# Performance work log

Measured on AMD Instinct MI355X. Metric: run time of the kernel, lower is better.

Reference implementation:

```python
import jax, jax.numpy as jnp
import numpy as np

K_BITS = 8
MOMENTUM = 0.125
EPS = 1e-05


def linear_quant(x, bits=K_BITS):
    """Dynamic-range fake quantization (LinearQuantFunction with dynamic=True).

    max_ = max(|x.max()|, |x.min()|), min_ = -max_, so zero_point = quant_max/2
    exactly, and nudged_zero_point = round(quant_max/2) (banker's rounding, as
    in Python's round()).
    """
    qmax = (1 << bits) - 1
    mx = jnp.maximum(jnp.abs(jnp.max(x)), jnp.abs(jnp.min(x)))
    scale = (2.0 * mx) / qmax  # range / quant_max
    nzp = float(round(qmax / 2))  # nudged zero point (constant under dynamic symmetric range)
    nmin = -nzp * scale
    nmax = (qmax - nzp) * scale
    safe = jnp.where(scale == 0, 1.0, scale)  # range==0 -> passthrough
    cs = jnp.clip(x, nmin, nmax) - nmin
    q = jnp.floor(cs / safe + 0.5) * safe + nmin
    return jnp.where(scale == 0, x, q)


def setup_inputs() -> dict:
    key = jax.random.key(0)
    k1, k2 = jax.random.split(key)
    N, C, H, W = 64, 256, 56, 56
    x = jax.random.normal(k1, (N, C, H, W), dtype=jnp.float32)
    weight = jax.random.uniform(k2, (C,), dtype=jnp.float32) - 0.5  # reset_parameters: U[0,1)-0.5
    bias = jnp.zeros((C,), dtype=jnp.float32)
    run_mean = jnp.zeros((C,), dtype=jnp.float32)
    run_var = jnp.ones((C,), dtype=jnp.float32)
    return {"x": x, "weight": weight, "bias": bias, "run_mean": run_mean, "run_var": run_var}


def reference(x, weight, bias, run_mean, run_var):
    # Training-mode forward of QuantizedBatchNorm (k=8 -> linear_quant path).
    q = linear_quant
    m = MOMENTUM
    bc = lambda v: v[None, :, None, None]  # per-channel broadcast over [N,C,H,W]

    # batch mean over all axes except channel (== _reorg(input).mean(1))
    new_mean = jnp.mean(x, axis=(0, 2, 3))
    mean = q((1.0 - m) * run_mean + m * new_mean)  # quantized updated running mean
    ctr = q(x - bc(mean))

    new_var = jnp.mean(ctr * ctr, axis=(0, 2, 3))
    var = q((1.0 - m) * run_var + m * new_var)  # quantized updated running var

    # quantizing the broadcast tensor == quantizing the per-channel vector,
    # since the quant scale depends only on the global max magnitude
    inv_den = q(jnp.sqrt(var + EPS))
    xn = q(ctr / bc(inv_den))

    qw = q(weight)
    qb = q(bias)  # bias==0 -> range 0 -> passthrough
    y = q(bc(qw) * xn + bc(qb))
    return y
```

## Files before the change

kernel.cpp:

```cpp
#include <hip/hip_runtime.h>
#include <stdint.h>


#define C_CH 256
#define P4 784
#define PLANE_STRIDE 200704
#define NHW_F 200704.0f
#define NHW_D 200704.0
#define TOLB 1e-3f

typedef float natf4 __attribute__((ext_vector_type(4)));

__device__ __forceinline__ float fq(float x, float sc, float qn, float qx) {
  if (sc == 0.0f) return x;
  float cs = __fsub_rn(fminf(fmaxf(x, qn), qx), qn);
  float f  = floorf(__fadd_rn(__fdiv_rn(cs, sc), 0.5f));
  return __fadd_rn(__fmul_rn(f, sc), qn);
}

__device__ __forceinline__ void qparams(float amax, float& sc, float& qn, float& qx) {
  sc = __fdiv_rn(__fmul_rn(2.0f, amax), 255.0f);
  qn = __fmul_rn(-128.0f, sc);
  qx = __fmul_rn(127.0f, sc);
}

__device__ __forceinline__ float block_max(float v, float* buf4) {
  #pragma unroll
  for (int m = 1; m <= 32; m <<= 1) v = fmaxf(v, __shfl_xor(v, m, 64));
  if ((threadIdx.x & 63) == 0) buf4[threadIdx.x >> 6] = v;
  __syncthreads();
  float r = fmaxf(fmaxf(buf4[0], buf4[1]), fmaxf(buf4[2], buf4[3]));
  __syncthreads();
  return r;
}

__device__ __forceinline__ uint32_t qlevel(float xv, float r2, float c2,
    float m, float s1, float n1, float x1) {
  float q = fmaf(xv, r2, c2);
  q = fminf(fmaxf(q, 0.0f), 255.0f);
  const float qh = __fadd_rn(q, 0.5f);
  float fl = floorf(qh);
  const float d = __fsub_rn(qh, fl);
  if (__builtin_expect(fminf(d, __fsub_rn(1.0f, d)) < TOLB, 0)) {
    const float tt = __fsub_rn(xv, m);
    const float cs = __fsub_rn(fminf(fmaxf(tt, n1), x1), n1);
    fl = floorf(__fadd_rn(__fdiv_rn(cs, s1), 0.5f));
  }
  return (uint32_t)fl;
}

struct S1Out { float meanc, tmax, tmin, s1, n1, x1; };

__device__ __forceinline__ void s1_compute(const float* __restrict__ psum,
    const float* __restrict__ pmin, const float* __restrict__ pmax,
    const float* __restrict__ run_mean, float* buf4, S1Out& o) {
  const int t = threadIdx.x;
  float sum = __fadd_rn(__fadd_rn(__fadd_rn(psum[4*t], psum[4*t+1]), psum[4*t+2]), psum[4*t+3]);
  float mn = fminf(fminf(pmin[4*t], pmin[4*t+1]), fminf(pmin[4*t+2], pmin[4*t+3]));
  float mx = fmaxf(fmaxf(pmax[4*t], pmax[4*t+1]), fmaxf(pmax[4*t+2], pmax[4*t+3]));
  const float new_mean = __fdiv_rn(sum, NHW_F);
  const float mp = __fadd_rn(__fmul_rn(0.875f, run_mean[t]), __fmul_rn(0.125f, new_mean));
  const float am = block_max(fabsf(mp), buf4);
  float scm, qnm, qxm; qparams(am, scm, qnm, qxm);
  o.meanc = fq(mp, scm, qnm, qxm);
  o.tmax = __fsub_rn(mx, o.meanc);
  o.tmin = __fsub_rn(mn, o.meanc);
  const float a1 = block_max(fmaxf(fabsf(o.tmax), fabsf(o.tmin)), buf4);
  qparams(a1, o.s1, o.n1, o.x1);
}

__global__ __launch_bounds__(256) void k_p1(const float4* __restrict__ x4,
    float* __restrict__ psum, float* __restrict__ pmin, float* __restrict__ pmax) {
  const int c = blockIdx.x, s = blockIdx.y, t = threadIdx.x;
  const int B0 = (s * 16 * C_CH + c) * P4;
  float sum = 0.0f, mn = INFINITY, mx = -INFINITY;
  #pragma unroll 1
  for (int g = 0; g < 7; ++g) {
    float4 v[7];
    #pragma unroll
    for (int j = 0; j < 7; ++j) {
      const int u = t + 256 * (7 * g + j);
      v[j] = x4[B0 + (u / P4) * PLANE_STRIDE + (u % P4)];
    }
    #pragma unroll
    for (int j = 0; j < 7; ++j) {
      const float4 w = v[j];
      sum = __fadd_rn(sum, __fadd_rn(__fadd_rn(w.x, w.y), __fadd_rn(w.z, w.w)));
      mn = fminf(mn, fminf(fminf(w.x, w.y), fminf(w.z, w.w)));
      mx = fmaxf(mx, fmaxf(fmaxf(w.x, w.y), fmaxf(w.z, w.w)));
    }
  }
  #pragma unroll
  for (int m = 1; m <= 32; m <<= 1) {
    sum = __fadd_rn(sum, __shfl_xor(sum, m, 64));
    mn = fminf(mn, __shfl_xor(mn, m, 64));
    mx = fmaxf(mx, __shfl_xor(mx, m, 64));
  }
  __shared__ float red[12];
  const int w_ = t >> 6;
  if ((t & 63) == 0) { red[w_] = sum; red[4 + w_] = mn; red[8 + w_] = mx; }
  __syncthreads();
  if (t == 0) {
    const int idx = c * 4 + s;
    psum[idx] = __fadd_rn(__fadd_rn(__fadd_rn(red[0], red[1]), red[2]), red[3]);
    pmin[idx] = fminf(fminf(red[4], red[5]), fminf(red[6], red[7]));
    pmax[idx] = fmaxf(fmaxf(red[8], red[9]), fmaxf(red[10], red[11]));
  }
}

__global__ __launch_bounds__(256) void k_p2(const float4* __restrict__ x4,
    const float* __restrict__ psum, const float* __restrict__ pmin,
    const float* __restrict__ pmax, const float* __restrict__ run_mean,
    uint32_t* __restrict__ pk, uint32_t* __restrict__ pk2) {
  __shared__ float buf4[4];
  __shared__ float bc[1];
  const int c = blockIdx.x, s = blockIdx.y, t = threadIdx.x;
  S1Out o; s1_compute(psum, pmin, pmax, run_mean, buf4, o);
  if (t == c) bc[0] = o.meanc;
  __syncthreads();
  const float m_c = bc[0];
  const double rd = 1.0 / (double)o.s1;
  const float r2 = (float)rd;
  const float c2 = (float)((-(double)m_c - (double)o.n1) * rd);
  const int B0 = (s * 16 * C_CH + c) * P4;
  int sk = 0, sk2 = 0;
  #pragma unroll 1
  for (int g = 0; g < 7; ++g) {
    float4 v[7];
    #pragma unroll
    for (int j = 0; j < 7; ++j) {
      const int u = t + 256 * (7 * g + j);
      v[j] = x4[B0 + (u / P4) * PLANE_STRIDE + (u % P4)];
    }
    #pragma unroll
    for (int j = 0; j < 7; ++j) {
      const float4 w = v[j];
      const float vv[4] = {w.x, w.y, w.z, w.w};
      #pragma unroll
      for (int e = 0; e < 4; ++e) {
        const uint32_t k = qlevel(vv[e], r2, c2, m_c, o.s1, o.n1, o.x1);
        sk += (int)k; sk2 += (int)(k * k);
      }
    }
  }
  #pragma unroll
  for (int m = 1; m <= 32; m <<= 1) {
    sk += __shfl_xor(sk, m, 64);
    sk2 += __shfl_xor(sk2, m, 64);
  }
  __shared__ uint32_t ired[8];
  const int w_ = t >> 6;
  if ((t & 63) == 0) { ired[w_] = (uint32_t)sk; ired[4 + w_] = (uint32_t)sk2; }
  __syncthreads();
  if (t == 0) {
    const int idx = c * 4 + s;
    pk[idx]  = ired[0] + ired[1] + ired[2] + ired[3];
    pk2[idx] = ired[4] + ired[5] + ired[6] + ired[7];
  }
}

__global__ __launch_bounds__(256) void k_p3(const float4* __restrict__ x4,
    const float* __restrict__ psum, const float* __restrict__ pmin,
    const float* __restrict__ pmax, const uint32_t* __restrict__ pk,
    const uint32_t* __restrict__ pk2,
    const float* __restrict__ run_mean, const float* __restrict__ run_var,
    const float* __restrict__ weight, const float* __restrict__ bias,
    natf4* __restrict__ y4) {
  __shared__ float buf4[4];
  __shared__ float bc[4];
  __shared__ float lut[256];
  const int c = blockIdx.x, s = blockIdx.y, t = threadIdx.x;
  S1Out o; s1_compute(psum, pmin, pmax, run_mean, buf4, o);
  const unsigned long long ssq = (unsigned long long)pk2[4*t] + pk2[4*t+1]
                               + pk2[4*t+2] + pk2[4*t+3];
  const unsigned int skc = pk[4*t] + pk[4*t+1] + pk[4*t+2] + pk[4*t+3];
  const double s1d = (double)o.s1;
  const double sum_ctr2 = s1d * s1d *
      ((double)ssq - 256.0 * (double)skc + 16384.0 * NHW_D);
  const float new_var = (float)(sum_ctr2 / NHW_D);
  const float vp = __fadd_rn(__fmul_rn(0.875f, run_var[t]), __fmul_rn(0.125f, new_var));
  const float av = block_max(fabsf(vp), buf4);
  float scv, qnv, qxv; qparams(av, scv, qnv, qxv);
  const float varc = fq(vp, scv, qnv, qxv);
  const float dp = __fsqrt_rn(__fadd_rn(varc, 1e-5f));
  const float ad = block_max(fabsf(dp), buf4);
  float scd, qnd, qxd; qparams(ad, scd, qnd, qxd);
  const float idc = fq(dp, scd, qnd, qxd);
  const float ctrmax = fq(o.tmax, o.s1, o.n1, o.x1);
  const float ctrmin = fq(o.tmin, o.s1, o.n1, o.x1);
  const float xpmax = __fdiv_rn(ctrmax, idc);
  const float xpmin = __fdiv_rn(ctrmin, idc);
  const float a3 = block_max(fmaxf(fabsf(xpmax), fabsf(xpmin)), buf4);
  float s3, n3, x3; qparams(a3, s3, n3, x3);
  const float xnmax = fq(xpmax, s3, n3, x3);
  const float xnmin = fq(xpmin, s3, n3, x3);
  const float wv = weight[t];
  const float aw = block_max(fabsf(wv), buf4);
  float scw, qnw, qxw; qparams(aw, scw, qnw, qxw);
  const float qw = fq(wv, scw, qnw, qxw);
  const float bv = bias[t];
  const float ab = block_max(fabsf(bv), buf4);
  float scb, qnb, qxb; qparams(ab, scb, qnb, qxb);
  const float qb = fq(bv, scb, qnb, qxb);
  const float e1 = __fadd_rn(__fmul_rn(qw, xnmax), qb);
  const float e2 = __fadd_rn(__fmul_rn(qw, xnmin), qb);
  const float a4 = block_max(fmaxf(fabsf(e1), fabsf(e2)), buf4);
  float s4, n4, x4q; qparams(a4, s4, n4, x4q);
  if (t == c) { bc[0] = idc; bc[1] = qw; bc[2] = qb; bc[3] = o.meanc; }
  __syncthreads();
  const float idc_c = bc[0], qw_c = bc[1], qb_c = bc[2], m_c = bc[3];
  {
    const float ctr_t = __fadd_rn(__fmul_rn((float)t, o.s1), o.n1);
    const float xn_t = fq(__fdiv_rn(ctr_t, idc_c), s3, n3, x3);
    lut[t] = fq(__fadd_rn(__fmul_rn(qw_c, xn_t), qb_c), s4, n4, x4q);
  }
  __syncthreads();

  const double rd = 1.0 / (double)o.s1;
  const float r2 = (float)rd;
  const float c2 = (float)((-(double)m_c - (double)o.n1) * rd);
  const int B0 = (s * 16 * C_CH + c) * P4;
  const float4* x4v = (const float4*)x4;
  #pragma unroll 1
  for (int g = 0; g < 7; ++g) {
    float4 v[7]; int idx[7];
    #pragma unroll
    for (int j = 0; j < 7; ++j) {
      const int u = t + 256 * (7 * g + j);
      idx[j] = B0 + (u / P4) * PLANE_STRIDE + (u % P4);
      v[j] = x4v[idx[j]];
    }
    #pragma unroll
    for (int j = 0; j < 7; ++j) {
      const float4 w = v[j];
      natf4 out;
      out.x = lut[qlevel(w.x, r2, c2, m_c, o.s1, o.n1, o.x1)];
      out.y = lut[qlevel(w.y, r2, c2, m_c, o.s1, o.n1, o.x1)];
      out.z = lut[qlevel(w.z, r2, c2, m_c, o.s1, o.n1, o.x1)];
      out.w = lut[qlevel(w.w, r2, c2, m_c, o.s1, o.n1, o.x1)];
      __builtin_nontemporal_store(out, &y4[idx[j]]);
    }
  }
}

extern "C" void kernel_launch(void* const* d_in, const int* in_sizes, int n_in,
                              void* d_out, int out_size, void* d_ws, size_t ws_size,
                              hipStream_t stream) {
  const float4* x4      = (const float4*)d_in[0];
  const float* weight   = (const float*)d_in[1];
  const float* bias     = (const float*)d_in[2];
  const float* run_mean = (const float*)d_in[3];
  const float* run_var  = (const float*)d_in[4];
  natf4* y4 = (natf4*)d_out;

  float* w = (float*)d_ws;
  float* psum = w;
  float* pmin = w + 1024;
  float* pmax = w + 2048;
  uint32_t* pk  = (uint32_t*)(w + 3072);
  uint32_t* pk2 = (uint32_t*)(w + 4096);

  dim3 grid(C_CH, 4), blk(256);
  k_p1<<<grid, blk, 0, stream>>>(x4, psum, pmin, pmax);
  k_p2<<<grid, blk, 0, stream>>>(x4, psum, pmin, pmax, run_mean, pk, pk2);
  k_p3<<<grid, blk, 0, stream>>>(x4, psum, pmin, pmax, pk, pk2,
                                 run_mean, run_var, weight, bias, y4);
}
```

Before: 134.6 us.

## Cache 8-bit quantization levels in workspace so the final pass skips re-reading x

The second pass now packs each element's 8-bit quantization level into a byte buffer in the workspace. The third pass reads these bytes and looks up the LUT instead of re-reading the fp32 input and recomputing qlevel. This replaces a 4-byte read per element in the last pass with a 1-byte write in pass 2 and a 1-byte read in pass 3, cutting total memory traffic. It needs about 51 MB of extra workspace and changes the loop mapping to 16 elements per thread slot.

```diff
diff --git a/kernel.cpp b/kernel.cpp
--- a/kernel.cpp
+++ b/kernel.cpp
@@ -4,7 +4,9 @@
 
 #define C_CH 256
 #define P4 784
+#define P16 196
 #define PLANE_STRIDE 200704
+#define KPLANE_STRIDE 50176
 #define NHW_F 200704.0f
 #define NHW_D 200704.0
 #define TOLB 1e-3f
@@ -69,108 +71,11 @@
   qparams(a1, o.s1, o.n1, o.x1);
 }
 
-__global__ __launch_bounds__(256) void k_p1(const float4* __restrict__ x4,
-    float* __restrict__ psum, float* __restrict__ pmin, float* __restrict__ pmax) {
-  const int c = blockIdx.x, s = blockIdx.y, t = threadIdx.x;
-  const int B0 = (s * 16 * C_CH + c) * P4;
-  float sum = 0.0f, mn = INFINITY, mx = -INFINITY;
-  #pragma unroll 1
-  for (int g = 0; g < 7; ++g) {
-    float4 v[7];
-    #pragma unroll
-    for (int j = 0; j < 7; ++j) {
-      const int u = t + 256 * (7 * g + j);
-      v[j] = x4[B0 + (u / P4) * PLANE_STRIDE + (u % P4)];
-    }
-    #pragma unroll
-    for (int j = 0; j < 7; ++j) {
-      const float4 w = v[j];
-      sum = __fadd_rn(sum, __fadd_rn(__fadd_rn(w.x, w.y), __fadd_rn(w.z, w.w)));
-      mn = fminf(mn, fminf(fminf(w.x, w.y), fminf(w.z, w.w)));
-      mx = fmaxf(mx, fmaxf(fmaxf(w.x, w.y), fmaxf(w.z, w.w)));
-    }
-  }
-  #pragma unroll
-  for (int m = 1; m <= 32; m <<= 1) {
-    sum = __fadd_rn(sum, __shfl_xor(sum, m, 64));
-    mn = fminf(mn, __shfl_xor(mn, m, 64));
-    mx = fmaxf(mx, __shfl_xor(mx, m, 64));
-  }
-  __shared__ float red[12];
-  const int w_ = t >> 6;
-  if ((t & 63) == 0) { red[w_] = sum; red[4 + w_] = mn; red[8 + w_] = mx; }
-  __syncthreads();
-  if (t == 0) {
-    const int idx = c * 4 + s;
-    psum[idx] = __fadd_rn(__fadd_rn(__fadd_rn(red[0], red[1]), red[2]), red[3]);
-    pmin[idx] = fminf(fminf(red[4], red[5]), fminf(red[6], red[7]));
-    pmax[idx] = fmaxf(fmaxf(red[8], red[9]), fmaxf(red[10], red[11]));
-  }
-}
-
-__global__ __launch_bounds__(256) void k_p2(const float4* __restrict__ x4,
-    const float* __restrict__ psum, const float* __restrict__ pmin,
-    const float* __restrict__ pmax, const float* __restrict__ run_mean,
-    uint32_t* __restrict__ pk, uint32_t* __restrict__ pk2) {
-  __shared__ float buf4[4];
-  __shared__ float bc[1];
-  const int c = blockIdx.x, s = blockIdx.y, t = threadIdx.x;
-  S1Out o; s1_compute(psum, pmin, pmax, run_mean, buf4, o);
-  if (t == c) bc[0] = o.meanc;
-  __syncthreads();
-  const float m_c = bc[0];
-  const double rd = 1.0 / (double)o.s1;
-  const float r2 = (float)rd;
-  const float c2 = (float)((-(double)m_c - (double)o.n1) * rd);
-  const int B0 = (s * 16 * C_CH + c) * P4;
-  int sk = 0, sk2 = 0;
-  #pragma unroll 1
-  for (int g = 0; g < 7; ++g) {
-    float4 v[7];
-    #pragma unroll
-    for (int j = 0; j < 7; ++j) {
-      const int u = t + 256 * (7 * g + j);
-      v[j] = x4[B0 + (u / P4) * PLANE_STRIDE + (u % P4)];
-    }
-    #pragma unroll
-    for (int j = 0; j < 7; ++j) {
-      const float4 w = v[j];
-      const float vv[4] = {w.x, w.y, w.z, w.w};
-      #pragma unroll
-      for (int e = 0; e < 4; ++e) {
-        const uint32_t k = qlevel(vv[e], r2, c2, m_c, o.s1, o.n1, o.x1);
-        sk += (int)k; sk2 += (int)(k * k);
-      }
-    }
-  }
-  #pragma unroll
-  for (int m = 1; m <= 32; m <<= 1) {
-    sk += __shfl_xor(sk, m, 64);
-    sk2 += __shfl_xor(sk2, m, 64);
-  }
-  __shared__ uint32_t ired[8];
-  const int w_ = t >> 6;
-  if ((t & 63) == 0) { ired[w_] = (uint32_t)sk; ired[4 + w_] = (uint32_t)sk2; }
-  __syncthreads();
-  if (t == 0) {
-    const int idx = c * 4 + s;
-    pk[idx]  = ired[0] + ired[1] + ired[2] + ired[3];
-    pk2[idx] = ired[4] + ired[5] + ired[6] + ired[7];
-  }
-}
-
-__global__ __launch_bounds__(256) void k_p3(const float4* __restrict__ x4,
-    const float* __restrict__ psum, const float* __restrict__ pmin,
-    const float* __restrict__ pmax, const uint32_t* __restrict__ pk,
-    const uint32_t* __restrict__ pk2,
-    const float* __restrict__ run_mean, const float* __restrict__ run_var,
-    const float* __restrict__ weight, const float* __restrict__ bias,
-    natf4* __restrict__ y4) {
-  __shared__ float buf4[4];
-  __shared__ float bc[4];
-  __shared__ float lut[256];
-  const int c = blockIdx.x, s = blockIdx.y, t = threadIdx.x;
-  S1Out o; s1_compute(psum, pmin, pmax, run_mean, buf4, o);
+__device__ __forceinline__ void s2_and_lut(const S1Out& o,
+    const uint32_t* __restrict__ pk, const uint32_t* __restrict__ pk2,
+    const float* __restrict__ run_var, const float* __restrict__ weight,
+    const float* __restrict__ bias, float* buf4, float* bc, float* lut, int c) {
+  const int t = threadIdx.x;
   const unsigned long long ssq = (unsigned long long)pk2[4*t] + pk2[4*t+1]
                                + pk2[4*t+2] + pk2[4*t+3];
   const unsigned int skc = pk[4*t] + pk[4*t+1] + pk[4*t+2] + pk[4*t+3];
@@ -206,39 +111,190 @@
   const float e2 = __fadd_rn(__fmul_rn(qw, xnmin), qb);
   const float a4 = block_max(fmaxf(fabsf(e1), fabsf(e2)), buf4);
   float s4, n4, x4q; qparams(a4, s4, n4, x4q);
-  if (t == c) { bc[0] = idc; bc[1] = qw; bc[2] = qb; bc[3] = o.meanc; }
-  __syncthreads();
-  const float idc_c = bc[0], qw_c = bc[1], qb_c = bc[2], m_c = bc[3];
-  {
-    const float ctr_t = __fadd_rn(__fmul_rn((float)t, o.s1), o.n1);
-    const float xn_t = fq(__fdiv_rn(ctr_t, idc_c), s3, n3, x3);
-    lut[t] = fq(__fadd_rn(__fmul_rn(qw_c, xn_t), qb_c), s4, n4, x4q);
-  }
-  __syncthreads();
-
+  if (t == c) { bc[0] = idc; bc[1] = qw; bc[2] = qb; }
+  __syncthreads();
+  const float idc_c = bc[0], qw_c = bc[1], qb_c = bc[2];
+  const float ctr_t = __fadd_rn(__fmul_rn((float)t, o.s1), o.n1);
+  const float xn_t = fq(__fdiv_rn(ctr_t, idc_c), s3, n3, x3);
+  lut[t] = fq(__fadd_rn(__fmul_rn(qw_c, xn_t), qb_c), s4, n4, x4q);
+  __syncthreads();
+}
+
+__global__ __launch_bounds__(256) void k_p1(const float4* __restrict__ x4,
+    float* __restrict__ psum, float* __restrict__ pmin, float* __restrict__ pmax) {
+  const int c = blockIdx.x, s = blockIdx.y, t = threadIdx.x;
+  const int B0 = (s * 16 * C_CH + c) * P4;
+  float sum = 0.0f, mn = INFINITY, mx = -INFINITY;
+  #pragma unroll 1
+  for (int g = 0; g < 7; ++g) {
+    float4 v[7];
+    #pragma unroll
+    for (int j = 0; j < 7; ++j) {
+      const int u = t + 256 * (7 * g + j);
+      v[j] = x4[B0 + (u / P4) * PLANE_STRIDE + (u % P4)];
+    }
+    #pragma unroll
+    for (int j = 0; j < 7; ++j) {
+      const float4 w = v[j];
+      sum = __fadd_rn(sum, __fadd_rn(__fadd_rn(w.x, w.y), __fadd_rn(w.z, w.w)));
+      mn = fminf(mn, fminf(fminf(w.x, w.y), fminf(w.z, w.w)));
+      mx = fmaxf(mx, fmaxf(fmaxf(w.x, w.y), fmaxf(w.z, w.w)));
+    }
+  }
+  #pragma unroll
+  for (int m = 1; m <= 32; m <<= 1) {
+    sum = __fadd_rn(sum, __shfl_xor(sum, m, 64));
+    mn = fminf(mn, __shfl_xor(mn, m, 64));
+    mx = fmaxf(mx, __shfl_xor(mx, m, 64));
+  }
+  __shared__ float red[12];
+  const int w_ = t >> 6;
+  if ((t & 63) == 0) { red[w_] = sum; red[4 + w_] = mn; red[8 + w_] = mx; }
+  __syncthreads();
+  if (t == 0) {
+    const int idx = c * 4 + s;
+    psum[idx] = __fadd_rn(__fadd_rn(__fadd_rn(red[0], red[1]), red[2]), red[3]);
+    pmin[idx] = fminf(fminf(red[4], red[5]), fminf(red[6], red[7]));
+    pmax[idx] = fmaxf(fmaxf(red[8], red[9]), fmaxf(red[10], red[11]));
+  }
+}
+
+__global__ __launch_bounds__(256) void k_p2(const float4* __restrict__ x4,
+    uint4* __restrict__ kq4,
+    const float* __restrict__ psum, const float* __restrict__ pmin,
+    const float* __restrict__ pmax, const float* __restrict__ run_mean,
+    uint32_t* __restrict__ pk, uint32_t* __restrict__ pk2) {
+  __shared__ float buf4[4];
+  __shared__ float bc[1];
+  const int c = blockIdx.x, s = blockIdx.y, t = threadIdx.x;
+  S1Out o; s1_compute(psum, pmin, pmax, run_mean, buf4, o);
+  if (t == c) bc[0] = o.meanc;
+  __syncthreads();
+  const float m_c = bc[0];
   const double rd = 1.0 / (double)o.s1;
   const float r2 = (float)rd;
   const float c2 = (float)((-(double)m_c - (double)o.n1) * rd);
   const int B0 = (s * 16 * C_CH + c) * P4;
-  const float4* x4v = (const float4*)x4;
+  const int KB0 = (s * 16 * C_CH + c) * P16;
+  int sk = 0, sk2 = 0;
   #pragma unroll 1
-  for (int g = 0; g < 7; ++g) {
-    float4 v[7]; int idx[7];
-    #pragma unroll
-    for (int j = 0; j < 7; ++j) {
-      const int u = t + 256 * (7 * g + j);
-      idx[j] = B0 + (u / P4) * PLANE_STRIDE + (u % P4);
-      v[j] = x4v[idx[j]];
-    }
-    #pragma unroll
-    for (int j = 0; j < 7; ++j) {
-      const float4 w = v[j];
+  for (int mm = 0; mm < 6; ++mm) {
+    float4 v[8]; int pl[2], sl[2];
+    #pragma unroll
+    for (int h = 0; h < 2; ++h) {
+      const int g = t + 256 * (2 * mm + h);
+      pl[h] = g / P16; sl[h] = g - pl[h] * P16;
+      const float4* p = x4 + B0 + pl[h] * PLANE_STRIDE + 4 * sl[h];
+      v[4*h+0] = p[0]; v[4*h+1] = p[1]; v[4*h+2] = p[2]; v[4*h+3] = p[3];
+    }
+    #pragma unroll
+    for (int h = 0; h < 2; ++h) {
+      uint32_t kw[4];
+      #pragma unroll
+      for (int q = 0; q < 4; ++q) {
+        const float4 w = v[4*h+q];
+        const float vv[4] = {w.x, w.y, w.z, w.w};
+        uint32_t acc = 0;
+        #pragma unroll
+        for (int e = 0; e < 4; ++e) {
+          const uint32_t k = qlevel(vv[e], r2, c2, m_c, o.s1, o.n1, o.x1);
+          sk += (int)k; sk2 += (int)(k * k);
+          acc |= k << (8 * e);
+        }
+        kw[q] = acc;
+      }
+      uint4 st; st.x = kw[0]; st.y = kw[1]; st.z = kw[2]; st.w = kw[3];
+      kq4[KB0 + pl[h] * KPLANE_STRIDE + sl[h]] = st;
+    }
+  }
+  if (t < 64) {
+    const int g = 3072 + t;
+    const int plane = g / P16, slot = g - plane * P16;
+    const float4* p = x4 + B0 + plane * PLANE_STRIDE + 4 * slot;
+    uint32_t kw[4];
+    #pragma unroll
+    for (int q = 0; q < 4; ++q) {
+      const float4 w = p[q];
+      const float vv[4] = {w.x, w.y, w.z, w.w};
+      uint32_t acc = 0;
+      #pragma unroll
+      for (int e = 0; e < 4; ++e) {
+        const uint32_t k = qlevel(vv[e], r2, c2, m_c, o.s1, o.n1, o.x1);
+        sk += (int)k; sk2 += (int)(k * k);
+        acc |= k << (8 * e);
+      }
+      kw[q] = acc;
+    }
+    uint4 st; st.x = kw[0]; st.y = kw[1]; st.z = kw[2]; st.w = kw[3];
+    kq4[KB0 + plane * KPLANE_STRIDE + slot] = st;
+  }
+  #pragma unroll
+  for (int m = 1; m <= 32; m <<= 1) {
+    sk += __shfl_xor(sk, m, 64);
+    sk2 += __shfl_xor(sk2, m, 64);
+  }
+  __shared__ uint32_t ired[8];
+  const int w_ = t >> 6;
+  if ((t & 63) == 0) { ired[w_] = (uint32_t)sk; ired[4 + w_] = (uint32_t)sk2; }
+  __syncthreads();
+  if (t == 0) {
+    const int idx = c * 4 + s;
+    pk[idx]  = ired[0] + ired[1] + ired[2] + ired[3];
+    pk2[idx] = ired[4] + ired[5] + ired[6] + ired[7];
+  }
+}
+
+__global__ __launch_bounds__(256) void k_p3(const uint4* __restrict__ kq4,
+    const float* __restrict__ psum, const float* __restrict__ pmin,
+    const float* __restrict__ pmax, const uint32_t* __restrict__ pk,
+    const uint32_t* __restrict__ pk2,
+    const float* __restrict__ run_mean, const float* __restrict__ run_var,
+    const float* __restrict__ weight, const float* __restrict__ bias,
+    natf4* __restrict__ y4) {
+  __shared__ float buf4[4];
+  __shared__ float bc[4];
+  __shared__ float lut[256];
+  const int c = blockIdx.x, s = blockIdx.y, t = threadIdx.x;
+  S1Out o; s1_compute(psum, pmin, pmax, run_mean, buf4, o);
+  s2_and_lut(o, pk, pk2, run_var, weight, bias, buf4, bc, lut, c);
+  const int B0 = (s * 16 * C_CH + c) * P4;
+  const int KB0 = (s * 16 * C_CH + c) * P16;
+  #pragma unroll 1
+  for (int mm = 0; mm < 6; ++mm) {
+    uint4 kk[2]; int pl[2], sl[2];
+    #pragma unroll
+    for (int h = 0; h < 2; ++h) {
+      const int g = t + 256 * (2 * mm + h);
+      pl[h] = g / P16; sl[h] = g - pl[h] * P16;
+      kk[h] = kq4[KB0 + pl[h] * KPLANE_STRIDE + sl[h]];
+    }
+    #pragma unroll
+    for (int h = 0; h < 2; ++h) {
+      natf4* yp = y4 + B0 + pl[h] * PLANE_STRIDE + 4 * sl[h];
+      const uint32_t ka[4] = {kk[h].x, kk[h].y, kk[h].z, kk[h].w};
+      #pragma unroll
+      for (int q = 0; q < 4; ++q) {
+        const uint32_t w = ka[q];
+        natf4 out;
+        out.x = lut[w & 255]; out.y = lut[(w >> 8) & 255];
+        out.z = lut[(w >> 16) & 255]; out.w = lut[w >> 24];
+        __builtin_nontemporal_store(out, &yp[q]);
+      }
+    }
+  }
+  if (t < 64) {
+    const int g = 3072 + t;
+    const int plane = g / P16, slot = g - plane * P16;
+    const uint4 kk = kq4[KB0 + plane * KPLANE_STRIDE + slot];
+    natf4* yp = y4 + B0 + plane * PLANE_STRIDE + 4 * slot;
+    const uint32_t ka[4] = {kk.x, kk.y, kk.z, kk.w};
+    #pragma unroll
+    for (int q = 0; q < 4; ++q) {
+      const uint32_t w = ka[q];
       natf4 out;
-      out.x = lut[qlevel(w.x, r2, c2, m_c, o.s1, o.n1, o.x1)];
-      out.y = lut[qlevel(w.y, r2, c2, m_c, o.s1, o.n1, o.x1)];
-      out.z = lut[qlevel(w.z, r2, c2, m_c, o.s1, o.n1, o.x1)];
-      out.w = lut[qlevel(w.w, r2, c2, m_c, o.s1, o.n1, o.x1)];
-      __builtin_nontemporal_store(out, &y4[idx[j]]);
+      out.x = lut[w & 255]; out.y = lut[(w >> 8) & 255];
+      out.z = lut[(w >> 16) & 255]; out.w = lut[w >> 24];
+      __builtin_nontemporal_store(out, &yp[q]);
     }
   }
 }
@@ -259,10 +315,11 @@
   float* pmax = w + 2048;
   uint32_t* pk  = (uint32_t*)(w + 3072);
   uint32_t* pk2 = (uint32_t*)(w + 4096);
+  uint4* kq4 = (uint4*)((char*)d_ws + 32768);
 
   dim3 grid(C_CH, 4), blk(256);
   k_p1<<<grid, blk, 0, stream>>>(x4, psum, pmin, pmax);
-  k_p2<<<grid, blk, 0, stream>>>(x4, psum, pmin, pmax, run_mean, pk, pk2);
-  k_p3<<<grid, blk, 0, stream>>>(x4, psum, pmin, pmax, pk, pk2,
+  k_p2<<<grid, blk, 0, stream>>>(x4, kq4, psum, pmin, pmax, run_mean, pk, pk2);
+  k_p3<<<grid, blk, 0, stream>>>(kq4, psum, pmin, pmax, pk, pk2,
                                  run_mean, run_var, weight, bias, y4);
 }
```

New measurement: 381.6 us. 2.84x slower.
